# Performance work log

Hardware: AMD Instinct MI355X
Metric: run time of the kernel (lower is better)

The kernel has to match this reference:

```python
import jax, jax.numpy as jnp
import numpy as np

BOS_ID = 0
EOS_ID = 1


def setup_inputs() -> dict:
    key = jax.random.key(0)
    ks = jax.random.split(key, 16)
    B, L, F = 64, 200, 512
    H, E, A = 512, 512, 512
    V, T = 50257, 21
    D = E + F  # rnn input_dim
    s = lambda n: 1.0 / np.sqrt(n)
    ref = jax.random.randint(ks[0], (B, T), 2, V, dtype=jnp.int32)
    ref = ref.at[:, 0].set(BOS_ID).at[:, -1].set(EOS_ID)
    return {
        "encoder_output": jax.random.normal(ks[1], (B, L, F), jnp.float32),
        "decoder_init_hidden": jax.random.normal(ks[2], (1, B, H), jnp.float32),
        "encoding_mask": jnp.ones((B, L, 1), jnp.float32),
        "temp_seg": jax.random.uniform(ks[3], (B, 2), jnp.float32),
        "embed_table": jax.random.normal(ks[4], (V, E), jnp.float32) * 0.02,
        "W_ih": jax.random.normal(ks[5], (3 * H, D), jnp.float32) * s(D),
        "W_hh": jax.random.normal(ks[6], (3 * H, H), jnp.float32) * s(H),
        "b_ih": jnp.zeros((3 * H,), jnp.float32),
        "b_hh": jnp.zeros((3 * H,), jnp.float32),
        "Wa_enc": jax.random.normal(ks[7], (F, A), jnp.float32) * s(F),
        "Wa_h": jax.random.normal(ks[8], (H, A), jnp.float32) * s(H),
        "v_att": jax.random.normal(ks[9], (A,), jnp.float32) * s(A),
        "W_out": jax.random.normal(ks[10], (V, H), jnp.float32) * s(H),
        "b_out": jnp.zeros((V,), jnp.float32),
        "ref_caption": ref,
    }


def reference(encoder_output, decoder_init_hidden, encoding_mask, temp_seg,
              embed_table, W_ih, W_hh, b_ih, b_hh,
              Wa_enc, Wa_h, v_att, W_out, b_out, ref_caption):
    # Teacher-forced training forward of RNNSeqDecoder (GRU, 1 layer).
    B, T = ref_caption.shape
    V = embed_table.shape[0]
    enc_proj = jnp.einsum('blf,fa->bla', encoder_output, Wa_enc)  # precompute attn enc term
    mask = encoding_mask[..., 0]  # (B,L)
    h0 = decoder_init_hidden[0]   # (B,H)

    def step(h, word):
        emb = embed_table[word]                                        # (B,E)
        # additive attention over encoder states (masked)
        score = jnp.einsum('bla,a->bl', jnp.tanh(enc_proj + (h @ Wa_h)[:, None, :]), v_att)
        score = jnp.where(mask > 0, score, -1e9)
        attn = jax.nn.softmax(score, axis=1)
        ctx = jnp.einsum('bl,blf->bf', attn, encoder_output)           # (B,F)
        x = jnp.concatenate([emb, ctx], axis=1)                        # (B,E+F)
        # PyTorch GRU cell
        gi = x @ W_ih.T + b_ih
        gh = h @ W_hh.T + b_hh
        i_r, i_z, i_n = jnp.split(gi, 3, axis=1)
        h_r, h_z, h_n = jnp.split(gh, 3, axis=1)
        r = jax.nn.sigmoid(i_r + h_r)
        z = jax.nn.sigmoid(i_z + h_z)
        n = jnp.tanh(i_n + r * h_n)
        h_new = (1.0 - z) * n + z * h
        logp = jax.nn.log_softmax(h_new @ W_out.T + b_out, axis=1)     # (B,V)
        return h_new, logp

    _, logps = jax.lax.scan(step, h0, ref_caption[:, :-1].T)           # (T-1,B,V)
    first = jnp.zeros((B, 1, V), logps.dtype)  # BOS_ID == 0, matches torch.zeros(...) + BOS_ID
    caption_prob = jnp.concatenate([first, jnp.swapaxes(logps, 0, 1)], axis=1)  # (B,T,V)
    return caption_prob
```

## Files before the change

kernel.cpp:

```cpp
#include <hip/hip_runtime.h>
#include <stdint.h>
#include <stddef.h>

#define B_ 64
#define L_ 200
#define F_ 512
#define H_ 512
#define A_ 512
#define E_ 512
#define V_ 50257
#define PADV 50304
#define T_ 21
#define D_ 1024
#define NBLK_LOG 786
#define BH (B_ * H_)
#define BD (B_ * D_)
#define NROW 1280

typedef __attribute__((ext_vector_type(8))) short short8;
typedef __attribute__((ext_vector_type(4))) float f32x4;

__device__ __forceinline__ unsigned short f2b(float f) {
  unsigned int u = __builtin_bit_cast(unsigned int, f);
  u += 0x7FFFu + ((u >> 16) & 1u);
  return (unsigned short)(u >> 16);
}
__device__ __forceinline__ float b2f(unsigned short s) {
  unsigned int u = ((unsigned int)s) << 16;
  return __builtin_bit_cast(float, u);
}
__device__ __forceinline__ f32x4 mfma16(short8 a, short8 b, f32x4 c) {
  return __builtin_amdgcn_mfma_f32_16x16x32_bf16(a, b, c, 0, 0, 0);
}
__device__ __forceinline__ int hsoff(int b, int j) {
  return (((b >> 4) * 16 + (j >> 5)) * 64 + (((j >> 3) & 3) * 16 + (b & 15))) * 8 + (j & 7);
}
__device__ __forceinline__ int xoff(int b, int k) {
  return (((b >> 4) * 32 + (k >> 5)) * 64 + (((k >> 3) & 3) * 16 + (b & 15))) * 8 + (k & 7);
}


__global__ void k_cvt(const float* __restrict__ src, unsigned short* __restrict__ dst, int n4) {
  int i = blockIdx.x * blockDim.x + threadIdx.x;
  int stride = gridDim.x * blockDim.x;
  const float4* s4 = (const float4*)src;
  ushort4* d4 = (ushort4*)dst;
  for (; i < n4; i += stride) {
    float4 v = s4[i];
    ushort4 o;
    o.x = f2b(v.x); o.y = f2b(v.y); o.z = f2b(v.z); o.w = f2b(v.w);
    d4[i] = o;
  }
}

__global__ void k_wfrag(const float* __restrict__ src, unsigned short* __restrict__ dst, int K) {
  int rt = blockIdx.x;
  int r15 = threadIdx.x & 15;
  int row = rt * 16 + r15;
  int nch = K >> 3;
  int kpw = K >> 5;
  for (int kc = threadIdx.x >> 4; kc < nch; kc += 16) {
    const float4* s = (const float4*)(src + (size_t)row * K + kc * 8);
    float4 x = s[0], y = s[1];
    short8 o;
    o[0] = f2b(x.x); o[1] = f2b(x.y); o[2] = f2b(x.z); o[3] = f2b(x.w);
    o[4] = f2b(y.x); o[5] = f2b(y.y); o[6] = f2b(y.z); o[7] = f2b(y.w);
    *(short8*)(dst + ((size_t)(rt * kpw + (kc >> 2)) * 64 + ((kc & 3) * 16 + r15)) * 8) = o;
  }
}

__global__ void k_transcvt(const float* __restrict__ src, unsigned short* __restrict__ dst, int R, int C) {
  __shared__ float tile[64][65];
  int cb = blockIdx.x * 64, rb = blockIdx.y * 64;
  int tx = threadIdx.x & 63, ty = threadIdx.x >> 6;
#pragma unroll
  for (int i = 0; i < 16; ++i) {
    int r = ty * 16 + i;
    tile[r][tx] = src[(size_t)(rb + r) * C + cb + tx];
  }
  __syncthreads();
#pragma unroll
  for (int i = 0; i < 16; ++i) {
    int c = ty * 16 + i;
    dst[(size_t)(cb + c) * R + rb + tx] = f2b(tile[tx][c]);
  }
}

__global__ void k_trans32(const float* __restrict__ src, float* __restrict__ dst, int R, int C) {
  __shared__ float tile[64][65];
  int cb = blockIdx.x * 64, rb = blockIdx.y * 64;
  int tx = threadIdx.x & 63, ty = threadIdx.x >> 6;
#pragma unroll
  for (int i = 0; i < 16; ++i) {
    int r = ty * 16 + i;
    tile[r][tx] = src[(size_t)(rb + r) * C + cb + tx];
  }
  __syncthreads();
#pragma unroll
  for (int i = 0; i < 16; ++i) {
    int c = ty * 16 + i;
    dst[(size_t)(cb + c) * R + rb + tx] = tile[tx][c];
  }
}

__global__ void k_hs0(const float* __restrict__ src, unsigned short* __restrict__ hs) {
  int b = blockIdx.x;
  for (int j = threadIdx.x; j < H_; j += 256)
    hs[hsoff(b, j)] = f2b(src[(size_t)b * H_ + j]);
}

__global__ void k_embAll(const int* __restrict__ ref, const float* __restrict__ et,
                         unsigned short* __restrict__ xAll) {
  int b = blockIdx.x, tp = blockIdx.y;
  int word = ref[b * T_ + tp];
  const float* er = et + (size_t)word * E_;
  unsigned short* dst = xAll + (size_t)tp * BD;
  int c = threadIdx.x;
  const float4* s = (const float4*)(er + c * 8);
  float4 x = s[0], y = s[1];
  short8 o;
  o[0] = f2b(x.x); o[1] = f2b(x.y); o[2] = f2b(x.z); o[3] = f2b(x.w);
  o[4] = f2b(y.x); o[5] = f2b(y.y); o[6] = f2b(y.z); o[7] = f2b(y.w);
  *(short8*)(dst + xoff(b, c * 8)) = o;
}

__global__ __launch_bounds__(256, 2) void k_encproj2(const unsigned short* __restrict__ encb,
                                                     const unsigned short* __restrict__ WaTb,
                                                     unsigned short* __restrict__ epb) {
  __shared__ unsigned short al[32768];
  int tid = threadIdx.x;
  size_t rowbase = (size_t)blockIdx.x * 64;
  for (int idx = tid; idx < 4096; idx += 256) {
    int row = idx >> 6, seg = idx & 63;
    unsigned char* dp = (unsigned char*)al + row * 1024 + ((seg * 16) ^ ((row & 7) << 4));
    *(short8*)dp = *(const short8*)(encb + (rowbase + row) * F_ + seg * 8);
  }
  __syncthreads();
  int w = tid >> 6, lane = tid & 63, ln15 = lane & 15, g = lane >> 4;
  int sw = (ln15 & 7) << 4;
  const unsigned char* alb = (const unsigned char*)al;
  int mrow = w * 16 + ln15;
  for (int nt = 0; nt < 32; ++nt) {
    f32x4 acc = {0.f, 0.f, 0.f, 0.f};
    const unsigned short* brow = WaTb + (size_t)(nt * 16 + ln15) * F_ + 8 * g;
#pragma unroll 4
    for (int kk = 0; kk < 16; ++kk) {
      short8 bf = *(const short8*)(brow + kk * 32);
      short8 af = *(const short8*)(alb + mrow * 1024 + ((kk * 64 + 16 * g) ^ sw));
      acc = mfma16(af, bf, acc);
    }
#pragma unroll
    for (int r = 0; r < 4; ++r) {
      size_t m = rowbase + w * 16 + 4 * g + r;
      epb[m * A_ + nt * 16 + ln15] = f2b(acc[r]);
    }
  }
}


__global__ __launch_bounds__(256) void k_hwgh(const unsigned short* __restrict__ Wahf,
                                              const unsigned short* __restrict__ Wfhh,
                                              const unsigned short* __restrict__ hs,
                                              float* __restrict__ hw,
                                              float* __restrict__ ghG) {
  int blk = blockIdx.x;
  int w = threadIdx.x >> 6, lane = threadIdx.x & 63;
  int ln15 = lane & 15, g = lane >> 4;
  if (blk < 32) {
    f32x4 acc = {0.f, 0.f, 0.f, 0.f};
#pragma unroll 4
    for (int kk = 0; kk < 16; ++kk) {
      short8 av = *(const short8*)(Wahf + (((size_t)blk * 16 + kk) * 64 + lane) * 8);
      short8 hv = *(const short8*)(hs + (((size_t)w * 16 + kk) * 64 + lane) * 8);
      acc = mfma16(av, hv, acc);
    }
#pragma unroll
    for (int r = 0; r < 4; ++r) {
      int a = blk * 16 + 4 * g + r;
      int b = w * 16 + ln15;
      hw[(size_t)b * 512 + a] = acc[r];
    }
  } else {
    int base = (blk - 32) * 3;
#pragma unroll
    for (int i = 0; i < 3; ++i) {
      int jt = base + i;
      f32x4 acc = {0.f, 0.f, 0.f, 0.f};
#pragma unroll
      for (int kk = 0; kk < 16; ++kk) {
        short8 wv = *(const short8*)(Wfhh + (((size_t)jt * 16 + kk) * 64 + lane) * 8);
        short8 hv = *(const short8*)(hs + (((size_t)w * 16 + kk) * 64 + lane) * 8);
        acc = mfma16(wv, hv, acc);
      }
#pragma unroll
      for (int r = 0; r < 4; ++r) {
        int j = jt * 16 + 4 * g + r;
        int b = w * 16 + ln15;
        ghG[(size_t)j * B_ + b] = acc[r];
      }
    }
  }
}


__global__ __launch_bounds__(1024) void k_attB(const float* __restrict__ mask,
                                               const float* __restrict__ vatt,
                                               const unsigned short* __restrict__ encb,
                                               const unsigned short* __restrict__ epb,
                                               const float* __restrict__ hw,
                                               unsigned short* __restrict__ xplane) {
  __shared__ float sm[208];
  __shared__ float ctxp[16][F_];
  __shared__ float ctxF[F_];
  int b = blockIdx.x;
  int tid = threadIdx.x;
  int w = tid >> 6, lane = tid & 63;
  float hwv[8], vv[8];
  {
    const float4* hp = (const float4*)(hw + (size_t)b * 512 + lane * 8);
    const float4* vp = (const float4*)(vatt + lane * 8);
    float4 h0 = hp[0], h1 = hp[1], v0 = vp[0], v1 = vp[1];
    hwv[0] = h0.x; hwv[1] = h0.y; hwv[2] = h0.z; hwv[3] = h0.w;
    hwv[4] = h1.x; hwv[5] = h1.y; hwv[6] = h1.z; hwv[7] = h1.w;
    vv[0] = v0.x; vv[1] = v0.y; vv[2] = v0.z; vv[3] = v0.w;
    vv[4] = v1.x; vv[5] = v1.y; vv[6] = v1.z; vv[7] = v1.w;
  }
  for (int l = w; l < L_; l += 16) {
    short8 ev = *(const short8*)(epb + ((size_t)(b * L_ + l)) * 512 + lane * 8);
    float p = 0.f;
#pragma unroll
    for (int j = 0; j < 8; ++j) {
      float x = b2f((unsigned short)ev[j]) + hwv[j];
      float e2 = __expf(x + x);
      p = fmaf(1.f - 2.f / (e2 + 1.f), vv[j], p);
    }
    for (int o = 1; o < 64; o <<= 1) p += __shfl_xor(p, o);
    if (lane == 0) {
      float mk = mask[b * L_ + l];
      sm[l] = (mk > 0.f) ? p : -1e9f;
    }
  }
  __syncthreads();
  if (tid < 64) {
    float m = -1e30f;
    for (int l = tid; l < L_; l += 64) m = fmaxf(m, sm[l]);
    for (int o = 1; o < 64; o <<= 1) m = fmaxf(m, __shfl_xor(m, o));
    float s = 0.f;
    for (int l = tid; l < L_; l += 64) s += __expf(sm[l] - m);
    for (int o = 1; o < 64; o <<= 1) s += __shfl_xor(s, o);
    float inv = 1.f / s;
    for (int l = tid; l < L_; l += 64) sm[l] = __expf(sm[l] - m) * inv;
  }
  __syncthreads();
  float c[8] = {0.f, 0.f, 0.f, 0.f, 0.f, 0.f, 0.f, 0.f};
  for (int l = w; l < L_; l += 16) {
    float wgt = sm[l];
    short8 ev = *(const short8*)(encb + ((size_t)(b * L_ + l)) * 512 + lane * 8);
#pragma unroll
    for (int j = 0; j < 8; ++j) c[j] = fmaf(wgt, b2f((unsigned short)ev[j]), c[j]);
  }
#pragma unroll
  for (int j = 0; j < 8; ++j) ctxp[w][lane * 8 + j] = c[j];
  __syncthreads();
  if (tid < 512) {
    float s = 0.f;
#pragma unroll
    for (int q = 0; q < 16; ++q) s += ctxp[q][tid];
    ctxF[tid] = s;
  }
  __syncthreads();
  if (tid < 64) {
    short8 o;
#pragma unroll
    for (int j = 0; j < 8; ++j) o[j] = f2b(ctxF[tid * 8 + j]);
    *(short8*)(xplane + xoff(b, E_ + tid * 8)) = o;
  }
}


__global__ __launch_bounds__(256) void k_stepB(const unsigned short* __restrict__ Wfih,
                                               const float* __restrict__ bih,
                                               const float* __restrict__ bhh,
                                               const unsigned short* __restrict__ xplane,
                                               const float* __restrict__ ghG,
                                               const float* __restrict__ hBold,
                                               unsigned short* __restrict__ hsnew,
                                               float* __restrict__ hBnew) {
  int bx = blockIdx.x;
  int w = threadIdx.x >> 6, lane = threadIdx.x & 63;
  int ln15 = lane & 15, g = lane >> 4;
  f32x4 z4 = {0.f, 0.f, 0.f, 0.f};
  f32x4 aIr = z4, aIz = z4, aIn = z4;
#pragma unroll 2
  for (int kk = 0; kk < 32; ++kk) {
    short8 xv = *(const short8*)(xplane + (((size_t)w * 32 + kk) * 64 + lane) * 8);
    aIr = mfma16(*(const short8*)(Wfih + (((size_t)(0 * 32 + bx) * 32 + kk) * 64 + lane) * 8), xv, aIr);
    aIz = mfma16(*(const short8*)(Wfih + (((size_t)(32 + bx) * 32 + kk) * 64 + lane) * 8), xv, aIz);
    aIn = mfma16(*(const short8*)(Wfih + (((size_t)(64 + bx) * 32 + kk) * 64 + lane) * 8), xv, aIn);
  }
  int jb = bx * 16;
#pragma unroll
  for (int r = 0; r < 4; ++r) {
    int j = jb + 4 * g + r;
    int b = w * 16 + ln15;
    float ir = aIr[r] + bih[j];
    float iz = aIz[r] + bih[512 + j];
    float in_ = aIn[r] + bih[1024 + j];
    float hrv = ghG[(size_t)j * B_ + b] + bhh[j];
    float hzv = ghG[(size_t)(512 + j) * B_ + b] + bhh[512 + j];
    float hnv = ghG[(size_t)(1024 + j) * B_ + b] + bhh[1024 + j];
    float rg = 1.f / (1.f + __expf(-(ir + hrv)));
    float zg = 1.f / (1.f + __expf(-(iz + hzv)));
    float e2 = __expf(2.f * (in_ + rg * hnv));
    float ng = 1.f - 2.f / (e2 + 1.f);
    float ho = hBold[(size_t)b * H_ + j];
    float hv = (1.f - zg) * ng + zg * ho;
    hBnew[(size_t)b * H_ + j] = hv;
    hsnew[hsoff(b, j)] = f2b(hv);
  }
}


__global__ __launch_bounds__(256) void k_blog(const unsigned short* __restrict__ Wb,
                                              const float* __restrict__ bout,
                                              const unsigned short* __restrict__ hsAll,
                                              float* __restrict__ out,
                                              unsigned short* __restrict__ lws, int mode) {
  __shared__ float tile[2][64][68];
  int tid = threadIdx.x;
  int w = tid >> 6, lane = tid & 63, ln15 = lane & 15, g = lane >> 4;
  int vcol = blockIdx.x * 64 + w * 16 + ln15;
  bool vok = vcol < V_;
  int vr = vok ? vcol : (V_ - 1);
  const unsigned short* brow = Wb + (size_t)vr * H_ + 8 * g;
  short8 wb[16];
#pragma unroll
  for (int kk = 0; kk < 16; ++kk) wb[kk] = *(const short8*)(brow + kk * 32);
  float bo = bout[vr];
  int row = tid >> 2, seg = tid & 3;

  for (int t = 0; t < T_ - 1; ++t) {
    const unsigned short* hp = hsAll + (size_t)(t + 1) * BH;
    int buf = t & 1;
    __builtin_amdgcn_s_setprio(1);
#pragma unroll
    for (int mp = 0; mp < 2; ++mp) {
      f32x4 z4 = {0.f, 0.f, 0.f, 0.f};
      f32x4 acc0 = z4, acc1 = z4;
#pragma unroll
      for (int kk = 0; kk < 16; ++kk) {
        short8 a0 = *(const short8*)(hp + (((mp * 2 + 0) * 16 + kk) * 64 + lane) * 8);
        short8 a1 = *(const short8*)(hp + (((mp * 2 + 1) * 16 + kk) * 64 + lane) * 8);
        acc0 = mfma16(a0, wb[kk], acc0);
        acc1 = mfma16(a1, wb[kk], acc1);
      }
#pragma unroll
      for (int r = 0; r < 4; ++r) {
        int bi0 = (mp * 2 + 0) * 16 + 4 * g + r;
        int bi1 = (mp * 2 + 1) * 16 + 4 * g + r;
        tile[buf][bi0][w * 16 + ln15] = vok ? acc0[r] + bo : -1e30f;
        tile[buf][bi1][w * 16 + ln15] = vok ? acc1[r] + bo : -1e30f;
      }
    }
    __builtin_amdgcn_s_setprio(0);
    __syncthreads();
    float v[16];
#pragma unroll
    for (int q = 0; q < 4; ++q) {
      float4 fv = *(const float4*)&tile[buf][row][seg * 16 + q * 4];
      v[q * 4 + 0] = fv.x; v[q * 4 + 1] = fv.y; v[q * 4 + 2] = fv.z; v[q * 4 + 3] = fv.w;
    }
    int cb = blockIdx.x * 64 + seg * 16;
    if (mode == 1) {
      unsigned short* orow = lws + ((size_t)t * 64 + row) * PADV + cb;
      short8 o0, o1;
#pragma unroll
      for (int i = 0; i < 8; ++i) { o0[i] = f2b(v[i]); o1[i] = f2b(v[8 + i]); }
      *(short8*)orow = o0;
      *(short8*)(orow + 8) = o1;
    } else {
      float* orow = out + ((size_t)row * T_ + (t + 1)) * V_ + cb;
      if (cb + 16 <= V_) {
#pragma unroll
        for (int q = 0; q < 4; ++q)
          *(float4*)(orow + q * 4) = make_float4(v[q * 4], v[q * 4 + 1], v[q * 4 + 2], v[q * 4 + 3]);
      } else {
        for (int i = 0; i < 16; ++i)
          if (cb + i < V_) orow[i] = v[i];
      }
    }
  }
}

__global__ __launch_bounds__(512) void k_lsefin(const unsigned short* __restrict__ lws,
                                                float* __restrict__ out) {
  __shared__ unsigned short srow[PADV];
  __shared__ float lm[512], ls[512];
  __shared__ float lvs;
  int bid = blockIdx.x;
  int tid = threadIdx.x;
  if (bid >= NROW) {
    int b = bid - NROW;
    float* o = out + (size_t)b * T_ * V_;
    float4 z = make_float4(0.f, 0.f, 0.f, 0.f);
    for (int i = tid; i < 12564; i += 512) *(float4*)(o + i * 4) = z;
    if (tid == 0) o[50256] = 0.f;
    return;
  }
  int rho = bid;
  int tp = rho >> 6, b = rho & 63;
  const unsigned short* src = lws + (size_t)(tp * 64 + b) * PADV;
  float* o = out + ((size_t)b * T_ + (tp + 1)) * V_;
  float m = -1e30f, s = 0.f;
  for (int i = tid; i < PADV / 8; i += 512) {
    short8 sv = *(const short8*)(src + i * 8);
    *(short8*)(srow + i * 8) = sv;
    float x0 = b2f((unsigned short)sv[0]), x1 = b2f((unsigned short)sv[1]);
    float x2 = b2f((unsigned short)sv[2]), x3 = b2f((unsigned short)sv[3]);
    float x4 = b2f((unsigned short)sv[4]), x5 = b2f((unsigned short)sv[5]);
    float x6 = b2f((unsigned short)sv[6]), x7 = b2f((unsigned short)sv[7]);
    float cm = fmaxf(fmaxf(fmaxf(x0, x1), fmaxf(x2, x3)), fmaxf(fmaxf(x4, x5), fmaxf(x6, x7)));
    float cs = __expf(x0 - cm) + __expf(x1 - cm) + __expf(x2 - cm) + __expf(x3 - cm) +
               __expf(x4 - cm) + __expf(x5 - cm) + __expf(x6 - cm) + __expf(x7 - cm);
    float nm = fmaxf(m, cm);
    s = s * __expf(m - nm) + cs * __expf(cm - nm);
    m = nm;
  }
  lm[tid] = m; ls[tid] = s;
  __syncthreads();
  for (int o2 = 256; o2 > 0; o2 >>= 1) {
    if (tid < o2) {
      float m2 = lm[tid + o2], s2 = ls[tid + o2];
      float nm = fmaxf(lm[tid], m2);
      ls[tid] = ls[tid] * __expf(lm[tid] - nm) + s2 * __expf(m2 - nm);
      lm[tid] = nm;
    }
    __syncthreads();
  }
  if (tid == 0) lvs = lm[0] + logf(ls[0]);
  __syncthreads();
  float Lv = lvs;
  for (int i = tid; i < 6282; i += 512) {
    short8 sv = *(const short8*)(srow + i * 8);
    float4 v0, v1;
    v0.x = b2f((unsigned short)sv[0]) - Lv; v0.y = b2f((unsigned short)sv[1]) - Lv;
    v0.z = b2f((unsigned short)sv[2]) - Lv; v0.w = b2f((unsigned short)sv[3]) - Lv;
    v1.x = b2f((unsigned short)sv[4]) - Lv; v1.y = b2f((unsigned short)sv[5]) - Lv;
    v1.z = b2f((unsigned short)sv[6]) - Lv; v1.w = b2f((unsigned short)sv[7]) - Lv;
    *(float4*)(o + i * 8) = v0;
    *(float4*)(o + i * 8 + 4) = v1;
  }
  if (tid == 0) o[50256] = b2f(srow[50256]) - Lv;
}

__global__ __launch_bounds__(256) void k_lsefin0(float* __restrict__ out) {
  __shared__ float lm[256], ls[256];
  __shared__ float lvs;
  int bid = blockIdx.x;
  int tid = threadIdx.x;
  if (bid >= NROW) {
    int b = bid - NROW;
    float* o = out + (size_t)b * T_ * V_;
    for (int v = tid; v < V_; v += 256) o[v] = 0.f;
    return;
  }
  int rho = bid;
  int tp = rho >> 6, b = rho & 63;
  float* o = out + ((size_t)b * T_ + (tp + 1)) * V_;
  float m = -1e30f, s = 0.f;
  for (int v = tid; v < V_; v += 256) {
    float x = o[v];
    float nm = fmaxf(m, x);
    s = s * __expf(m - nm) + __expf(x - nm);
    m = nm;
  }
  lm[tid] = m; ls[tid] = s;
  __syncthreads();
  for (int o2 = 128; o2 > 0; o2 >>= 1) {
    if (tid < o2) {
      float m2 = lm[tid + o2], s2 = ls[tid + o2];
      float nm = fmaxf(lm[tid], m2);
      ls[tid] = ls[tid] * __expf(lm[tid] - nm) + s2 * __expf(m2 - nm);
      lm[tid] = nm;
    }
    __syncthreads();
  }
  if (tid == 0) lvs = lm[0] + logf(ls[0]);
  __syncthreads();
  float Lv = lvs;
  for (int v = tid; v < V_; v += 256) o[v] -= Lv;
}


extern "C" void kernel_launch(void* const* d_in, const int* in_sizes, int n_in,
                              void* d_out, int out_size, void* d_ws, size_t ws_size,
                              hipStream_t stream) {
  const float* enc   = (const float*)d_in[0];
  const float* dih   = (const float*)d_in[1];
  const float* mask  = (const float*)d_in[2];
  const float* et    = (const float*)d_in[4];
  const float* Wih   = (const float*)d_in[5];
  const float* Whh   = (const float*)d_in[6];
  const float* bih   = (const float*)d_in[7];
  const float* bhh   = (const float*)d_in[8];
  const float* Waenc = (const float*)d_in[9];
  const float* Wah   = (const float*)d_in[10];
  const float* vatt  = (const float*)d_in[11];
  const float* Wout  = (const float*)d_in[12];
  const float* bout  = (const float*)d_in[13];
  const int*   ref   = (const int*)d_in[14];
  float* out = (float*)d_out;

  char* w = (char*)d_ws;
  size_t o = 0;
  unsigned short* Wb    = (unsigned short*)(w + o); o += (size_t)V_ * H_ * 2;
  unsigned short* Wfih  = (unsigned short*)(w + o); o += (size_t)1536 * 1024 * 2;
  unsigned short* Wfhh  = (unsigned short*)(w + o); o += (size_t)1536 * 512 * 2;
  unsigned short* WaTb  = (unsigned short*)(w + o); o += (size_t)512 * 512 * 2;
  unsigned short* Wahf  = (unsigned short*)(w + o); o += (size_t)512 * 512 * 2;
  float* WahT32 = (float*)(w + o); o += (size_t)512 * 512 * 4;
  unsigned short* encb  = (unsigned short*)(w + o); o += (size_t)B_ * L_ * F_ * 2;
  unsigned short* epb   = (unsigned short*)(w + o); o += (size_t)B_ * L_ * A_ * 2;
  unsigned short* xAll  = (unsigned short*)(w + o); o += (size_t)20 * BD * 2;
  unsigned short* hsAll = (unsigned short*)(w + o); o += (size_t)T_ * BH * 2;
  float* hBAll = (float*)(w + o); o += (size_t)T_ * BH * 4;
  float* ghG   = (float*)(w + o); o += (size_t)1536 * B_ * 4;
  float* hw    = (float*)(w + o); o += (size_t)B_ * A_ * 4 + 256;
  unsigned short* lws = (unsigned short*)(w + o);
  size_t need = o + (size_t)NROW * PADV * 2;
  int mode = (ws_size >= need) ? 1 : 0;

  k_cvt<<<4096, 256, 0, stream>>>(Wout, Wb, V_ * H_ / 4);
  k_cvt<<<2048, 256, 0, stream>>>(enc, encb, B_ * L_ * F_ / 4);
  k_wfrag<<<96, 256, 0, stream>>>(Wih, Wfih, 1024);
  k_wfrag<<<96, 256, 0, stream>>>(Whh, Wfhh, 512);
  k_transcvt<<<dim3(8, 8), 256, 0, stream>>>(Waenc, WaTb, 512, 512);
  k_trans32<<<dim3(8, 8), 256, 0, stream>>>(Wah, WahT32, 512, 512);
  k_wfrag<<<32, 256, 0, stream>>>(WahT32, Wahf, 512);
  k_hs0<<<64, 256, 0, stream>>>(dih, hsAll);
  k_embAll<<<dim3(64, 20), 64, 0, stream>>>(ref, et, xAll);
  k_encproj2<<<200, 256, 0, stream>>>(encb, WaTb, epb);

  for (int t = 0; t < T_ - 1; ++t) {
    const float* hB_t = (t == 0) ? dih : (hBAll + (size_t)t * BH);
    float* hB_n = hBAll + (size_t)(t + 1) * BH;
    const unsigned short* hs_t = hsAll + (size_t)t * BH;
    unsigned short* hs_n = hsAll + (size_t)(t + 1) * BH;
    unsigned short* xp = xAll + (size_t)t * BD;
    k_hwgh<<<64, 256, 0, stream>>>(Wahf, Wfhh, hs_t, hw, ghG);
    k_attB<<<64, 1024, 0, stream>>>(mask, vatt, encb, epb, hw, xp);
    k_stepB<<<32, 256, 0, stream>>>(Wfih, bih, bhh, xp, ghG, hB_t, hs_n, hB_n);
  }
  k_blog<<<NBLK_LOG, 256, 0, stream>>>(Wb, bout, hsAll, out, lws, mode);
  if (mode == 1) k_lsefin<<<NROW + 64, 512, 0, stream>>>(lws, out);
  else k_lsefin0<<<NROW + 64, 256, 0, stream>>>(out);
}
```

Baseline: 1.356 ms.

## Fuse hidden-projection GEMVs into attention and GRU kernels, drop k_hwgh launch

Result: slower. 1.594 ms (+17.6%).

```diff
diff --git a/kernel.cpp b/kernel.cpp
--- a/kernel.cpp
+++ b/kernel.cpp
@@ -158,70 +158,44 @@
 }
 
 
-__global__ __launch_bounds__(256) void k_hwgh(const unsigned short* __restrict__ Wahf,
-                                              const unsigned short* __restrict__ Wfhh,
-                                              const unsigned short* __restrict__ hs,
-                                              float* __restrict__ hw,
-                                              float* __restrict__ ghG) {
-  int blk = blockIdx.x;
-  int w = threadIdx.x >> 6, lane = threadIdx.x & 63;
-  int ln15 = lane & 15, g = lane >> 4;
-  if (blk < 32) {
-    f32x4 acc = {0.f, 0.f, 0.f, 0.f};
-#pragma unroll 4
-    for (int kk = 0; kk < 16; ++kk) {
-      short8 av = *(const short8*)(Wahf + (((size_t)blk * 16 + kk) * 64 + lane) * 8);
-      short8 hv = *(const short8*)(hs + (((size_t)w * 16 + kk) * 64 + lane) * 8);
-      acc = mfma16(av, hv, acc);
-    }
-#pragma unroll
-    for (int r = 0; r < 4; ++r) {
-      int a = blk * 16 + 4 * g + r;
-      int b = w * 16 + ln15;
-      hw[(size_t)b * 512 + a] = acc[r];
-    }
-  } else {
-    int base = (blk - 32) * 3;
-#pragma unroll
-    for (int i = 0; i < 3; ++i) {
-      int jt = base + i;
-      f32x4 acc = {0.f, 0.f, 0.f, 0.f};
-#pragma unroll
-      for (int kk = 0; kk < 16; ++kk) {
-        short8 wv = *(const short8*)(Wfhh + (((size_t)jt * 16 + kk) * 64 + lane) * 8);
-        short8 hv = *(const short8*)(hs + (((size_t)w * 16 + kk) * 64 + lane) * 8);
-        acc = mfma16(wv, hv, acc);
-      }
-#pragma unroll
-      for (int r = 0; r < 4; ++r) {
-        int j = jt * 16 + 4 * g + r;
-        int b = w * 16 + ln15;
-        ghG[(size_t)j * B_ + b] = acc[r];
-      }
-    }
-  }
-}
-
-
-__global__ __launch_bounds__(1024) void k_attB(const float* __restrict__ mask,
-                                               const float* __restrict__ vatt,
-                                               const unsigned short* __restrict__ encb,
-                                               const unsigned short* __restrict__ epb,
-                                               const float* __restrict__ hw,
-                                               unsigned short* __restrict__ xplane) {
+__global__ __launch_bounds__(1024) void k_attB2(const float* __restrict__ mask,
+                                                const float* __restrict__ vatt,
+                                                const unsigned short* __restrict__ encb,
+                                                const unsigned short* __restrict__ epb,
+                                                const unsigned short* __restrict__ Wahf,
+                                                const unsigned short* __restrict__ hs,
+                                                unsigned short* __restrict__ xplane) {
+  __shared__ float Shw[A_];
   __shared__ float sm[208];
   __shared__ float ctxp[16][F_];
   __shared__ float ctxF[F_];
   int b = blockIdx.x;
   int tid = threadIdx.x;
   int w = tid >> 6, lane = tid & 63;
+  int ln15 = lane & 15, g = lane >> 4;
+  int bg = b >> 4, bl = b & 15;
+#pragma unroll
+  for (int q = 0; q < 2; ++q) {
+    int nt = w + q * 16;
+    f32x4 acc = {0.f, 0.f, 0.f, 0.f};
+#pragma unroll 4
+    for (int kk = 0; kk < 16; ++kk) {
+      short8 av = *(const short8*)(Wahf + (((size_t)nt * 16 + kk) * 64 + lane) * 8);
+      short8 hv = *(const short8*)(hs + (((size_t)bg * 16 + kk) * 64 + lane) * 8);
+      acc = mfma16(av, hv, acc);
+    }
+    if (ln15 == bl) {
+#pragma unroll
+      for (int r = 0; r < 4; ++r) Shw[nt * 16 + 4 * g + r] = acc[r];
+    }
+  }
+  __syncthreads();
   float hwv[8], vv[8];
+#pragma unroll
+  for (int j = 0; j < 8; ++j) hwv[j] = Shw[lane * 8 + j];
   {
-    const float4* hp = (const float4*)(hw + (size_t)b * 512 + lane * 8);
     const float4* vp = (const float4*)(vatt + lane * 8);
-    float4 h0 = hp[0], h1 = hp[1], v0 = vp[0], v1 = vp[1];
-    hwv[0] = h0.x; hwv[1] = h0.y; hwv[2] = h0.z; hwv[3] = h0.w;
-    hwv[4] = h1.x; hwv[5] = h1.y; hwv[6] = h1.z; hwv[7] = h1.w;
+    float4 v0 = vp[0], v1 = vp[1];
     vv[0] = v0.x; vv[1] = v0.y; vv[2] = v0.z; vv[3] = v0.w;
     vv[4] = v1.x; vv[5] = v1.y; vv[6] = v1.z; vv[7] = v1.w;
   }
@@ -278,11 +252,12 @@
 }
 
 
-__global__ __launch_bounds__(256) void k_stepB(const unsigned short* __restrict__ Wfih,
+__global__ __launch_bounds__(256) void k_gruM2(const unsigned short* __restrict__ Wfih,
+                                               const unsigned short* __restrict__ Wfhh,
                                                const float* __restrict__ bih,
                                                const float* __restrict__ bhh,
                                                const unsigned short* __restrict__ xplane,
-                                               const float* __restrict__ ghG,
+                                               const unsigned short* __restrict__ hsold,
                                                const float* __restrict__ hBold,
                                                unsigned short* __restrict__ hsnew,
                                                float* __restrict__ hBnew) {
@@ -290,13 +265,24 @@
   int w = threadIdx.x >> 6, lane = threadIdx.x & 63;
   int ln15 = lane & 15, g = lane >> 4;
   f32x4 z4 = {0.f, 0.f, 0.f, 0.f};
-  f32x4 aIr = z4, aIz = z4, aIn = z4;
+  f32x4 aIr = z4, aIz = z4, aIn = z4, aHr = z4, aHz = z4, aHn = z4;
+  {
 #pragma unroll 2
-  for (int kk = 0; kk < 32; ++kk) {
-    short8 xv = *(const short8*)(xplane + (((size_t)w * 32 + kk) * 64 + lane) * 8);
-    aIr = mfma16(*(const short8*)(Wfih + (((size_t)(0 * 32 + bx) * 32 + kk) * 64 + lane) * 8), xv, aIr);
-    aIz = mfma16(*(const short8*)(Wfih + (((size_t)(32 + bx) * 32 + kk) * 64 + lane) * 8), xv, aIz);
-    aIn = mfma16(*(const short8*)(Wfih + (((size_t)(64 + bx) * 32 + kk) * 64 + lane) * 8), xv, aIn);
+    for (int kk = 0; kk < 32; ++kk) {
+      short8 xv = *(const short8*)(xplane + (((size_t)w * 32 + kk) * 64 + lane) * 8);
+      aIr = mfma16(*(const short8*)(Wfih + (((size_t)(0 * 32 + bx) * 32 + kk) * 64 + lane) * 8), xv, aIr);
+      aIz = mfma16(*(const short8*)(Wfih + (((size_t)(32 + bx) * 32 + kk) * 64 + lane) * 8), xv, aIz);
+      aIn = mfma16(*(const short8*)(Wfih + (((size_t)(64 + bx) * 32 + kk) * 64 + lane) * 8), xv, aIn);
+    }
+  }
+  {
+#pragma unroll 2
+    for (int kk = 0; kk < 16; ++kk) {
+      short8 hv = *(const short8*)(hsold + (((size_t)w * 16 + kk) * 64 + lane) * 8);
+      aHr = mfma16(*(const short8*)(Wfhh + (((size_t)(0 * 32 + bx) * 16 + kk) * 64 + lane) * 8), hv, aHr);
+      aHz = mfma16(*(const short8*)(Wfhh + (((size_t)(32 + bx) * 16 + kk) * 64 + lane) * 8), hv, aHz);
+      aHn = mfma16(*(const short8*)(Wfhh + (((size_t)(64 + bx) * 16 + kk) * 64 + lane) * 8), hv, aHn);
+    }
   }
   int jb = bx * 16;
 #pragma unroll
@@ -306,9 +292,9 @@
     float ir = aIr[r] + bih[j];
     float iz = aIz[r] + bih[512 + j];
     float in_ = aIn[r] + bih[1024 + j];
-    float hrv = ghG[(size_t)j * B_ + b] + bhh[j];
-    float hzv = ghG[(size_t)(512 + j) * B_ + b] + bhh[512 + j];
-    float hnv = ghG[(size_t)(1024 + j) * B_ + b] + bhh[1024 + j];
+    float hrv = aHr[r] + bhh[j];
+    float hzv = aHz[r] + bhh[512 + j];
+    float hnv = aHn[r] + bhh[1024 + j];
     float rg = 1.f / (1.f + __expf(-(ir + hrv)));
     float zg = 1.f / (1.f + __expf(-(iz + hzv)));
     float e2 = __expf(2.f * (in_ + rg * hnv));
@@ -391,6 +377,7 @@
     }
   }
 }
+
 
 __global__ __launch_bounds__(512) void k_lsefin(const unsigned short* __restrict__ lws,
                                                 float* __restrict__ out) {
@@ -523,9 +510,7 @@
   unsigned short* epb   = (unsigned short*)(w + o); o += (size_t)B_ * L_ * A_ * 2;
   unsigned short* xAll  = (unsigned short*)(w + o); o += (size_t)20 * BD * 2;
   unsigned short* hsAll = (unsigned short*)(w + o); o += (size_t)T_ * BH * 2;
-  float* hBAll = (float*)(w + o); o += (size_t)T_ * BH * 4;
-  float* ghG   = (float*)(w + o); o += (size_t)1536 * B_ * 4;
-  float* hw    = (float*)(w + o); o += (size_t)B_ * A_ * 4 + 256;
+  float* hBAll = (float*)(w + o); o += (size_t)T_ * BH * 4 + 256;
   unsigned short* lws = (unsigned short*)(w + o);
   size_t need = o + (size_t)NROW * PADV * 2;
   int mode = (ws_size >= need) ? 1 : 0;
@@ -547,9 +532,8 @@
     const unsigned short* hs_t = hsAll + (size_t)t * BH;
     unsigned short* hs_n = hsAll + (size_t)(t + 1) * BH;
     unsigned short* xp = xAll + (size_t)t * BD;
-    k_hwgh<<<64, 256, 0, stream>>>(Wahf, Wfhh, hs_t, hw, ghG);
-    k_attB<<<64, 1024, 0, stream>>>(mask, vatt, encb, epb, hw, xp);
-    k_stepB<<<32, 256, 0, stream>>>(Wfih, bih, bhh, xp, ghG, hB_t, hs_n, hB_n);
+    k_attB2<<<64, 1024, 0, stream>>>(mask, vatt, encb, epb, Wahf, hs_t, xp);
+    k_gruM2<<<32, 256, 0, stream>>>(Wfih, Wfhh, bih, bhh, xp, hs_t, hB_t, hs_n, hB_n);
   }
   k_blog<<<NBLK_LOG, 256, 0, stream>>>(Wb, bout, hsAll, out, lws, mode);
   if (mode == 1) k_lsefin<<<NROW + 64, 512, 0, stream>>>(lws, out);
```

## Merge setup kernels into two launches and spread hidden GEMM over more blocks

Applied to the files above, without the earlier changes.

New measurement: 1.320 ms. 1.03x faster.

```diff
diff --git a/kernel.cpp b/kernel.cpp
--- a/kernel.cpp
+++ b/kernel.cpp
@@ -40,9 +40,10 @@
 }
 
 
-__global__ void k_cvt(const float* __restrict__ src, unsigned short* __restrict__ dst, int n4) {
-  int i = blockIdx.x * blockDim.x + threadIdx.x;
-  int stride = gridDim.x * blockDim.x;
+__device__ void cvt_dev(const float* __restrict__ src, unsigned short* __restrict__ dst,
+                        int n4, int vbid, int nblk) {
+  int i = vbid * 256 + threadIdx.x;
+  int stride = nblk * 256;
   const float4* s4 = (const float4*)src;
   ushort4* d4 = (ushort4*)dst;
   for (; i < n4; i += stride) {
@@ -53,8 +54,8 @@
   }
 }
 
-__global__ void k_wfrag(const float* __restrict__ src, unsigned short* __restrict__ dst, int K) {
-  int rt = blockIdx.x;
+__device__ void wfrag_dev(const float* __restrict__ src, unsigned short* __restrict__ dst,
+                          int K, int rt) {
   int r15 = threadIdx.x & 15;
   int row = rt * 16 + r15;
   int nch = K >> 3;
@@ -69,67 +70,91 @@
   }
 }
 
-__global__ void k_transcvt(const float* __restrict__ src, unsigned short* __restrict__ dst, int R, int C) {
+__global__ __launch_bounds__(256) void k_setupA(const float* __restrict__ Wout, unsigned short* __restrict__ Wb,
+                                                const float* __restrict__ enc, unsigned short* __restrict__ encb,
+                                                const float* __restrict__ Wih, unsigned short* __restrict__ Wfih,
+                                                const float* __restrict__ Whh, unsigned short* __restrict__ Wfhh,
+                                                const float* __restrict__ Waenc, unsigned short* __restrict__ WaTb,
+                                                const float* __restrict__ Wah, float* __restrict__ WahT32,
+                                                const float* __restrict__ dih, unsigned short* __restrict__ hsAll,
+                                                const int* __restrict__ ref, const float* __restrict__ et,
+                                                unsigned short* __restrict__ xAll) {
   __shared__ float tile[64][65];
-  int cb = blockIdx.x * 64, rb = blockIdx.y * 64;
-  int tx = threadIdx.x & 63, ty = threadIdx.x >> 6;
-#pragma unroll
-  for (int i = 0; i < 16; ++i) {
-    int r = ty * 16 + i;
-    tile[r][tx] = src[(size_t)(rb + r) * C + cb + tx];
-  }
-  __syncthreads();
-#pragma unroll
-  for (int i = 0; i < 16; ++i) {
-    int c = ty * 16 + i;
-    dst[(size_t)(cb + c) * R + rb + tx] = f2b(tile[tx][c]);
-  }
-}
-
-__global__ void k_trans32(const float* __restrict__ src, float* __restrict__ dst, int R, int C) {
-  __shared__ float tile[64][65];
-  int cb = blockIdx.x * 64, rb = blockIdx.y * 64;
-  int tx = threadIdx.x & 63, ty = threadIdx.x >> 6;
-#pragma unroll
-  for (int i = 0; i < 16; ++i) {
-    int r = ty * 16 + i;
-    tile[r][tx] = src[(size_t)(rb + r) * C + cb + tx];
-  }
-  __syncthreads();
-#pragma unroll
-  for (int i = 0; i < 16; ++i) {
-    int c = ty * 16 + i;
-    dst[(size_t)(cb + c) * R + rb + tx] = tile[tx][c];
-  }
-}
-
-__global__ void k_hs0(const float* __restrict__ src, unsigned short* __restrict__ hs) {
-  int b = blockIdx.x;
-  for (int j = threadIdx.x; j < H_; j += 256)
-    hs[hsoff(b, j)] = f2b(src[(size_t)b * H_ + j]);
-}
-
-__global__ void k_embAll(const int* __restrict__ ref, const float* __restrict__ et,
-                         unsigned short* __restrict__ xAll) {
-  int b = blockIdx.x, tp = blockIdx.y;
-  int word = ref[b * T_ + tp];
-  const float* er = et + (size_t)word * E_;
-  unsigned short* dst = xAll + (size_t)tp * BD;
-  int c = threadIdx.x;
-  const float4* s = (const float4*)(er + c * 8);
-  float4 x = s[0], y = s[1];
-  short8 o;
-  o[0] = f2b(x.x); o[1] = f2b(x.y); o[2] = f2b(x.z); o[3] = f2b(x.w);
-  o[4] = f2b(y.x); o[5] = f2b(y.y); o[6] = f2b(y.z); o[7] = f2b(y.w);
-  *(short8*)(dst + xoff(b, c * 8)) = o;
-}
-
-__global__ __launch_bounds__(256, 2) void k_encproj2(const unsigned short* __restrict__ encb,
-                                                     const unsigned short* __restrict__ WaTb,
-                                                     unsigned short* __restrict__ epb) {
+  int bid = blockIdx.x;
+  int tid = threadIdx.x;
+  if (bid < 4096) {
+    cvt_dev(Wout, Wb, V_ * H_ / 4, bid, 4096);
+  } else if (bid < 6144) {
+    cvt_dev(enc, encb, B_ * L_ * F_ / 4, bid - 4096, 2048);
+  } else if (bid < 6240) {
+    wfrag_dev(Wih, Wfih, 1024, bid - 6144);
+  } else if (bid < 6336) {
+    wfrag_dev(Whh, Wfhh, 512, bid - 6240);
+  } else if (bid < 6400) {
+    int q = bid - 6336;
+    int cb = (q & 7) * 64, rb = (q >> 3) * 64;
+    int tx = tid & 63, ty = tid >> 6;
+#pragma unroll
+    for (int i = 0; i < 16; ++i) {
+      int r = ty * 16 + i;
+      tile[r][tx] = Waenc[(size_t)(rb + r) * 512 + cb + tx];
+    }
+    __syncthreads();
+#pragma unroll
+    for (int i = 0; i < 16; ++i) {
+      int c = ty * 16 + i;
+      WaTb[(size_t)(cb + c) * 512 + rb + tx] = f2b(tile[tx][c]);
+    }
+  } else if (bid < 6464) {
+    int q = bid - 6400;
+    int cb = (q & 7) * 64, rb = (q >> 3) * 64;
+    int tx = tid & 63, ty = tid >> 6;
+#pragma unroll
+    for (int i = 0; i < 16; ++i) {
+      int r = ty * 16 + i;
+      tile[r][tx] = Wah[(size_t)(rb + r) * 512 + cb + tx];
+    }
+    __syncthreads();
+#pragma unroll
+    for (int i = 0; i < 16; ++i) {
+      int c = ty * 16 + i;
+      WahT32[(size_t)(cb + c) * 512 + rb + tx] = tile[tx][c];
+    }
+  } else if (bid < 6528) {
+    int b = bid - 6464;
+    for (int j = tid; j < H_; j += 256)
+      hsAll[hsoff(b, j)] = f2b(dih[(size_t)b * H_ + j]);
+  } else {
+    int q = bid - 6528;
+    int b = q & 63, tp = q >> 6;
+    if (tid < 64) {
+      int word = ref[b * T_ + tp];
+      const float* er = et + (size_t)word * E_;
+      unsigned short* dst = xAll + (size_t)tp * BD;
+      int c = tid;
+      const float4* s = (const float4*)(er + c * 8);
+      float4 x = s[0], y = s[1];
+      short8 o;
+      o[0] = f2b(x.x); o[1] = f2b(x.y); o[2] = f2b(x.z); o[3] = f2b(x.w);
+      o[4] = f2b(y.x); o[5] = f2b(y.y); o[6] = f2b(y.z); o[7] = f2b(y.w);
+      *(short8*)(dst + xoff(b, c * 8)) = o;
+    }
+  }
+}
+
+__global__ __launch_bounds__(256) void k_setupB(const float* __restrict__ WahT32,
+                                                unsigned short* __restrict__ Wahf,
+                                                const unsigned short* __restrict__ encb,
+                                                const unsigned short* __restrict__ WaTb,
+                                                unsigned short* __restrict__ epb) {
   __shared__ unsigned short al[32768];
+  int bid = blockIdx.x;
   int tid = threadIdx.x;
-  size_t rowbase = (size_t)blockIdx.x * 64;
+  if (bid < 32) {
+    wfrag_dev(WahT32, Wahf, 512, bid);
+    return;
+  }
+  size_t rowbase = (size_t)(bid - 32) * 64;
   for (int idx = tid; idx < 4096; idx += 256) {
     int row = idx >> 6, seg = idx & 63;
     unsigned char* dp = (unsigned char*)al + row * 1024 + ((seg * 16) ^ ((row & 7) << 4));
@@ -181,23 +206,19 @@
       hw[(size_t)b * 512 + a] = acc[r];
     }
   } else {
-    int base = (blk - 32) * 3;
-#pragma unroll
-    for (int i = 0; i < 3; ++i) {
-      int jt = base + i;
-      f32x4 acc = {0.f, 0.f, 0.f, 0.f};
-#pragma unroll
-      for (int kk = 0; kk < 16; ++kk) {
-        short8 wv = *(const short8*)(Wfhh + (((size_t)jt * 16 + kk) * 64 + lane) * 8);
-        short8 hv = *(const short8*)(hs + (((size_t)w * 16 + kk) * 64 + lane) * 8);
-        acc = mfma16(wv, hv, acc);
-      }
-#pragma unroll
-      for (int r = 0; r < 4; ++r) {
-        int j = jt * 16 + 4 * g + r;
-        int b = w * 16 + ln15;
-        ghG[(size_t)j * B_ + b] = acc[r];
-      }
+    int jt = blk - 32;
+    f32x4 acc = {0.f, 0.f, 0.f, 0.f};
+#pragma unroll
+    for (int kk = 0; kk < 16; ++kk) {
+      short8 wv = *(const short8*)(Wfhh + (((size_t)jt * 16 + kk) * 64 + lane) * 8);
+      short8 hv = *(const short8*)(hs + (((size_t)w * 16 + kk) * 64 + lane) * 8);
+      acc = mfma16(wv, hv, acc);
+    }
+#pragma unroll
+    for (int r = 0; r < 4; ++r) {
+      int j = jt * 16 + 4 * g + r;
+      int b = w * 16 + ln15;
+      ghG[(size_t)j * B_ + b] = acc[r];
     }
   }
 }
@@ -392,6 +413,7 @@
   }
 }
 
+
 __global__ __launch_bounds__(512) void k_lsefin(const unsigned short* __restrict__ lws,
                                                 float* __restrict__ out) {
   __shared__ unsigned short srow[PADV];
@@ -530,16 +552,9 @@
   size_t need = o + (size_t)NROW * PADV * 2;
   int mode = (ws_size >= need) ? 1 : 0;
 
-  k_cvt<<<4096, 256, 0, stream>>>(Wout, Wb, V_ * H_ / 4);
-  k_cvt<<<2048, 256, 0, stream>>>(enc, encb, B_ * L_ * F_ / 4);
-  k_wfrag<<<96, 256, 0, stream>>>(Wih, Wfih, 1024);
-  k_wfrag<<<96, 256, 0, stream>>>(Whh, Wfhh, 512);
-  k_transcvt<<<dim3(8, 8), 256, 0, stream>>>(Waenc, WaTb, 512, 512);
-  k_trans32<<<dim3(8, 8), 256, 0, stream>>>(Wah, WahT32, 512, 512);
-  k_wfrag<<<32, 256, 0, stream>>>(WahT32, Wahf, 512);
-  k_hs0<<<64, 256, 0, stream>>>(dih, hsAll);
-  k_embAll<<<dim3(64, 20), 64, 0, stream>>>(ref, et, xAll);
-  k_encproj2<<<200, 256, 0, stream>>>(encb, WaTb, epb);
+  k_setupA<<<7808, 256, 0, stream>>>(Wout, Wb, enc, encb, Wih, Wfih, Whh, Wfhh,
+                                     Waenc, WaTb, Wah, WahT32, dih, hsAll, ref, et, xAll);
+  k_setupB<<<232, 256, 0, stream>>>(WahT32, Wahf, encb, WaTb, epb);
 
   for (int t = 0; t < T_ - 1; ++t) {
     const float* hB_t = (t == 0) ? dih : (hBAll + (size_t)t * BH);
@@ -547,7 +562,7 @@
     const unsigned short* hs_t = hsAll + (size_t)t * BH;
     unsigned short* hs_n = hsAll + (size_t)(t + 1) * BH;
     unsigned short* xp = xAll + (size_t)t * BD;
-    k_hwgh<<<64, 256, 0, stream>>>(Wahf, Wfhh, hs_t, hw, ghG);
+    k_hwgh<<<128, 256, 0, stream>>>(Wahf, Wfhh, hs_t, hw, ghG);
     k_attB<<<64, 1024, 0, stream>>>(mask, vatt, encb, epb, hw, xp);
     k_stepB<<<32, 256, 0, stream>>>(Wfih, bih, bhh, xp, ghG, hB_t, hs_n, hB_n);
   }
```
